# Kernel tuning notes

Hardware: AMD Instinct MI355X
Metric: run time of the kernel (lower is better)

The kernel has to match this reference:

```python
import jax, jax.numpy as jnp
import numpy as np

W_BIT = 4
G_SIZE = 128
HID = 4096
INTER = 11008
TOKS = (2, 2048)


def _dequant(qw, qz, scales, g_size):
    """Unpack int4 nibbles from int32 and dequantize: (w - zero) * scale.
    qw: [K, N//8] int32, qz: [K//g, N//8] int32, scales: [K//g, N] float.
    Returns dense weight [K, N] in scales.dtype."""
    K = qw.shape[0]
    shifts = (jnp.arange(8, dtype=jnp.int32) * 4)  # 8 nibbles per int32
    w = ((qw[:, :, None] >> shifts) & 0xF).reshape(K, -1).astype(scales.dtype)   # [K, N]
    z = ((qz[:, :, None] >> shifts) & 0xF).reshape(qz.shape[0], -1).astype(scales.dtype)  # [K//g, N]
    zr = jnp.repeat(z, g_size, axis=0)       # broadcast zero-points over group rows
    sr = jnp.repeat(scales, g_size, axis=0)  # broadcast scales over group rows
    return (w - zr) * sr


def setup_inputs() -> dict:
    key = jax.random.key(0)
    ks = jax.random.split(key, 7)
    B, S = TOKS
    x = jax.random.normal(ks[0], (B, S, HID), dtype=jnp.float32)
    imax = 2147483647
    qweight_gu = jax.random.randint(ks[1], (HID, 2 * INTER // 8), 0, imax, dtype=jnp.int32)
    qzeros_gu = jax.random.randint(ks[2], (HID // G_SIZE, 2 * INTER // 8), 0, imax, dtype=jnp.int32)
    scales_gu = jax.random.uniform(ks[3], (HID // G_SIZE, 2 * INTER), dtype=jnp.float32) * 0.01 + 1e-3
    qweight_dn = jax.random.randint(ks[4], (INTER, HID // 8), 0, imax, dtype=jnp.int32)
    qzeros_dn = jax.random.randint(ks[5], (INTER // G_SIZE, HID // 8), 0, imax, dtype=jnp.int32)
    scales_dn = jax.random.uniform(ks[6], (INTER // G_SIZE, HID), dtype=jnp.float32) * 0.01 + 1e-3
    return {"x": x, "qweight_gu": qweight_gu, "qzeros_gu": qzeros_gu, "scales_gu": scales_gu,
            "qweight_dn": qweight_dn, "qzeros_dn": qzeros_dn, "scales_dn": scales_dn}


def reference(x, qweight_gu, qzeros_gu, scales_gu, qweight_dn, qzeros_dn, scales_dn):
    # gate_up projection: x [B,S,H] @ W_gu [H, 2*I]
    W_gu = _dequant(qweight_gu, qzeros_gu, scales_gu, G_SIZE)
    gate_up = jnp.einsum('bsh,hi->bsi', x, W_gu)
    d = gate_up.shape[-1] // 2
    # SiluAndMul: silu(gate) * up
    h = jax.nn.silu(gate_up[..., :d]) * gate_up[..., d:]
    # down projection: h [B,S,I] @ W_dn [I, H]
    W_dn = _dequant(qweight_dn, qzeros_dn, scales_dn, G_SIZE)
    return jnp.einsum('bsi,ih->bsh', h, W_dn)
```

## Files before the change

kernel.cpp:

```cpp
#include <hip/hip_runtime.h>
#include <hip/hip_bf16.h>
#include <cstdint>
#include <cstddef>

#define AS1 __attribute__((address_space(1)))
#define AS3 __attribute__((address_space(3)))

constexpr int HIDC   = 4096;
constexpr int INTERC = 11008;
constexpr int NTOKC  = 4096;
constexpr int NWGU   = 2 * INTERC;

using f32x4 = __attribute__((ext_vector_type(4))) float;
using s16x8 = __attribute__((ext_vector_type(8))) short;

__device__ __forceinline__ short f2bf(float f) {
  __hip_bfloat16 h = __float2bfloat16(f);
  return __builtin_bit_cast(short, h);
}


__global__ void cvt_x_kernel(const float4* __restrict__ x, ushort4* __restrict__ xb, int n4) {
  int stride = gridDim.x * blockDim.x;
  for (int i = blockIdx.x * blockDim.x + threadIdx.x; i < n4; i += stride) {
    float4 v = x[i];
    ushort4 o;
    o.x = (unsigned short)f2bf(v.x);
    o.y = (unsigned short)f2bf(v.y);
    o.z = (unsigned short)f2bf(v.z);
    o.w = (unsigned short)f2bf(v.w);
    xb[i] = o;
  }
}

__global__ void repack_kernel(const uint32_t* __restrict__ qw, uint32_t* __restrict__ qt,
                              int kints, int Wn) {
  long total  = (long)Wn * kints;
  long stride = (long)gridDim.x * blockDim.x;
  for (long idx = blockIdx.x * (long)blockDim.x + threadIdx.x; idx < total; idx += stride) {
    int col = (int)(idx / kints);
    int kk  = (int)(idx - (long)col * kints);
    uint32_t ow[8] = {0, 0, 0, 0, 0, 0, 0, 0};
#pragma unroll
    for (int j = 0; j < 8; ++j) {
      uint32_t v = qw[(size_t)(kk * 8 + j) * Wn + col];
#pragma unroll
      for (int jn = 0; jn < 8; ++jn)
        ow[jn] |= ((v >> (4 * jn)) & 0xFu) << (4 * j);
    }
#pragma unroll
    for (int jn = 0; jn < 8; ++jn)
      qt[(size_t)(col * 8 + jn) * kints + kk] = ow[jn];
  }
}

__global__ void mktab_kernel(const uint32_t* __restrict__ qz, const float* __restrict__ sc,
                             float2* __restrict__ tab, int total, int Nw) {
  int stride = gridDim.x * blockDim.x;
  for (int idx = blockIdx.x * blockDim.x + threadIdx.x; idx < total; idx += stride) {
    int g = idx / Nw, n = idx - g * Nw;
    uint32_t z = (qz[(size_t)g * (Nw >> 3) + (n >> 3)] >> ((n & 7) * 4)) & 0xFu;
    float s = sc[idx];
    tab[idx] = make_float2(s, -s * (float)z);
  }
}

template <int DUAL, int KSTEPS, int KINTS, int NWTOT>
__global__ __launch_bounds__(256, 2) void qgemm_kernel(
    const __hip_bfloat16* __restrict__ A, const uint32_t* __restrict__ QT,
    const float2* __restrict__ TAB, __hip_bfloat16* __restrict__ Hout,
    float* __restrict__ Fout) {
  constexpr int K  = KSTEPS * 64;
  constexpr int NI = DUAL ? 2 : 4;
  __shared__ __align__(16) char lds[32768];

  const int tid  = threadIdx.x;
  const int lane = tid & 63;
  const int w    = tid >> 6;
  const int wr   = w >> 1, wc = w & 1;
  const int fr   = lane & 15;
  const int fq   = lane >> 4;
  const int nt   = blockIdx.x, mt = blockIdx.y;
  const int row0 = mt * 128;

  int a_src[4];
#pragma unroll
  for (int i = 0; i < 4; ++i) {
    int o = i * 4096 + tid * 16;
    int r = o >> 7;
    int b = (o & 127) ^ ((r & 7) << 4);
    a_src[i] = (row0 + r) * K + (b >> 1);
  }

  int s_mat, s_nl, s_kh, s_nglob;
  if (DUAL) {
    s_mat = tid >> 7;
    int tt = tid & 127;
    s_nl  = tt >> 1;
    s_kh  = tt & 1;
    s_nglob = nt * 64 + s_nl + (s_mat ? INTERC : 0);
  } else {
    s_mat = 0;
    s_nl  = tid >> 1;
    s_kh  = tid & 1;
    s_nglob = nt * 128 + s_nl;
  }
  char* bdst = lds + 16384 + s_mat * 8192 + s_nl * 128;
  const int bswz = (s_nl & 7) << 4;

  f32x4 acc0[4][NI] = {};
  f32x4 acc1[4][NI] = {};

#pragma unroll 1
  for (int kt = 0; kt < KSTEPS; ++kt) {
    if (kt) __syncthreads();

#pragma unroll
    for (int i = 0; i < 4; ++i) {
      const __hip_bfloat16* src = A + a_src[i] + kt * 64;
      __builtin_amdgcn_global_load_lds((const AS1 uint32_t*)src,
                                       (AS3 uint32_t*)(lds + i * 4096 + w * 1024),
                                       16, 0, 0);
    }

    {
      const int g = kt >> 1;
      const uint32_t* qp = QT + (size_t)s_nglob * KINTS + kt * 8 + s_kh * 4;
      uint4 q = *(const uint4*)qp;
      float2 sz = TAB[(size_t)g * NWTOT + s_nglob];
      uint32_t qq[4] = {q.x, q.y, q.z, q.w};
#pragma unroll
      for (int ii = 0; ii < 4; ++ii) {
        s16x8 wv;
#pragma unroll
        for (int j = 0; j < 8; ++j) {
          float v = (float)((qq[ii] >> (4 * j)) & 0xFu);
          wv[j] = f2bf(fmaf(v, sz.x, sz.y));
        }
        *(s16x8*)(bdst + ((s_kh * 64 + ii * 16) ^ bswz)) = wv;
      }
    }
    __syncthreads();

#pragma unroll
    for (int kk = 0; kk < 2; ++kk) {
      const int bb = (((kk << 2) | fq) ^ (fr & 7)) << 4;
      s16x8 av[4];
#pragma unroll
      for (int mi = 0; mi < 4; ++mi)
        av[mi] = *(const s16x8*)(lds + (wr * 64 + mi * 16 + fr) * 128 + bb);
      if (DUAL) {
#pragma unroll
        for (int ni = 0; ni < 2; ++ni) {
          const int brow = (wc * 32 + ni * 16 + fr) * 128 + bb;
          s16x8 bg = *(const s16x8*)(lds + 16384 + brow);
          s16x8 bu = *(const s16x8*)(lds + 24576 + brow);
#pragma unroll
          for (int mi = 0; mi < 4; ++mi) {
            acc0[mi][ni] = __builtin_amdgcn_mfma_f32_16x16x32_bf16(av[mi], bg, acc0[mi][ni], 0, 0, 0);
            acc1[mi][ni] = __builtin_amdgcn_mfma_f32_16x16x32_bf16(av[mi], bu, acc1[mi][ni], 0, 0, 0);
          }
        }
      } else {
#pragma unroll
        for (int ni = 0; ni < 4; ++ni) {
          s16x8 bv = *(const s16x8*)(lds + 16384 + (wc * 64 + ni * 16 + fr) * 128 + bb);
#pragma unroll
          for (int mi = 0; mi < 4; ++mi)
            acc0[mi][ni] = __builtin_amdgcn_mfma_f32_16x16x32_bf16(av[mi], bv, acc0[mi][ni], 0, 0, 0);
        }
      }
    }
  }

  if (DUAL) {
    const int col0 = nt * 64 + wc * 32;
#pragma unroll
    for (int mi = 0; mi < 4; ++mi) {
      const int rr = row0 + wr * 64 + mi * 16 + fq * 4;
#pragma unroll
      for (int ni = 0; ni < NI; ++ni) {
        const int cc = col0 + ni * 16 + fr;
#pragma unroll
        for (int r = 0; r < 4; ++r) {
          float gv = acc0[mi][ni][r];
          float uv = acc1[mi][ni][r];
          float hv = gv / (1.0f + __expf(-gv)) * uv;
          Hout[(size_t)(rr + r) * INTERC + cc] = __float2bfloat16(hv);
        }
      }
    }
  } else {
    const int col0 = nt * 128 + wc * 64;
#pragma unroll
    for (int mi = 0; mi < 4; ++mi) {
      const int rr = row0 + wr * 64 + mi * 16 + fq * 4;
#pragma unroll
      for (int ni = 0; ni < NI; ++ni) {
        const int cc = col0 + ni * 16 + fr;
#pragma unroll
        for (int r = 0; r < 4; ++r)
          Fout[(size_t)(rr + r) * HIDC + cc] = acc0[mi][ni][r];
      }
    }
  }
}

extern "C" void kernel_launch(void* const* d_in, const int* in_sizes, int n_in,
                              void* d_out, int out_size, void* d_ws, size_t ws_size,
                              hipStream_t stream) {
  const float*    x     = (const float*)d_in[0];
  const uint32_t* qw_gu = (const uint32_t*)d_in[1];
  const uint32_t* qz_gu = (const uint32_t*)d_in[2];
  const float*    sc_gu = (const float*)d_in[3];
  const uint32_t* qw_dn = (const uint32_t*)d_in[4];
  const uint32_t* qz_dn = (const uint32_t*)d_in[5];
  const float*    sc_dn = (const float*)d_in[6];
  float* out = (float*)d_out;

  char* ws = (char*)d_ws;
  __hip_bfloat16* xb   = (__hip_bfloat16*)(ws + 0);
  uint32_t*       qtgu = (uint32_t*)(ws + 33554432);
  uint32_t*       qtdn = (uint32_t*)(ws + 78643200);
  float2*         tgu  = (float2*)(ws + 101187584);
  float2*         tdn  = (float2*)(ws + 106823680);
  __hip_bfloat16* hbuf = (__hip_bfloat16*)(ws + 109641728);

  cvt_x_kernel<<<2048, 256, 0, stream>>>((const float4*)x, (ushort4*)xb, NTOKC * HIDC / 4);
  repack_kernel<<<2048, 256, 0, stream>>>(qw_gu, qtgu, HIDC / 8, NWGU / 8);
  repack_kernel<<<2048, 256, 0, stream>>>(qw_dn, qtdn, INTERC / 8, HIDC / 8);
  mktab_kernel<<<1024, 256, 0, stream>>>(qz_gu, sc_gu, tgu, (HIDC / 128) * NWGU, NWGU);
  mktab_kernel<<<1024, 256, 0, stream>>>(qz_dn, sc_dn, tdn, (INTERC / 128) * HIDC, HIDC);

  qgemm_kernel<1, 64, 512, NWGU>
      <<<dim3(INTERC / 64, NTOKC / 128), 256, 0, stream>>>(xb, qtgu, tgu, hbuf, nullptr);
  qgemm_kernel<0, 172, 1376, HIDC>
      <<<dim3(HIDC / 128, NTOKC / 128), 256, 0, stream>>>(hbuf, qtdn, tdn, nullptr, out);
}
```

Before: 1.323 ms.

## Switch GEMMs to fp16 with magic-number packed int4 dequantization

Moves activations, the intermediate buffer and the dequantized weights from bf16 to fp16 and uses the f16 MFMA. The repack now interleaves nibbles so that each 32-bit word can be split into packed half2 pairs with the 0x6400 magic-exponent trick. Dequantization then becomes a half2 subtract and a half2 fma, replacing eight scalar int-to-float conversions, fmas and bf16 conversions per word. The scale/zero table is stored as duplicated half2 pairs. The aim is to cut VALU cost in the B-tile dequant path. The cost is fp16 range limits: the intermediate h values or the scale times zero term could overflow or lose precision.

```diff
diff --git a/kernel.cpp b/kernel.cpp
--- a/kernel.cpp
+++ b/kernel.cpp
@@ -1,5 +1,6 @@
 #include <hip/hip_runtime.h>
 #include <hip/hip_bf16.h>
+#include <hip/hip_fp16.h>
 #include <cstdint>
 #include <cstddef>
 
@@ -12,24 +13,19 @@
 constexpr int NWGU   = 2 * INTERC;
 
 using f32x4 = __attribute__((ext_vector_type(4))) float;
-using s16x8 = __attribute__((ext_vector_type(8))) short;
-
-__device__ __forceinline__ short f2bf(float f) {
-  __hip_bfloat16 h = __float2bfloat16(f);
-  return __builtin_bit_cast(short, h);
-}
-
-
-__global__ void cvt_x_kernel(const float4* __restrict__ x, ushort4* __restrict__ xb, int n4) {
+using f16x8 = __attribute__((ext_vector_type(8))) _Float16;
+
+
+__global__ void cvt_x_kernel(const float4* __restrict__ x, ushort4* __restrict__ xh, int n4) {
   int stride = gridDim.x * blockDim.x;
   for (int i = blockIdx.x * blockDim.x + threadIdx.x; i < n4; i += stride) {
     float4 v = x[i];
     ushort4 o;
-    o.x = (unsigned short)f2bf(v.x);
-    o.y = (unsigned short)f2bf(v.y);
-    o.z = (unsigned short)f2bf(v.z);
-    o.w = (unsigned short)f2bf(v.w);
-    xb[i] = o;
+    o.x = __builtin_bit_cast(unsigned short, __float2half(v.x));
+    o.y = __builtin_bit_cast(unsigned short, __float2half(v.y));
+    o.z = __builtin_bit_cast(unsigned short, __float2half(v.z));
+    o.w = __builtin_bit_cast(unsigned short, __float2half(v.w));
+    xh[i] = o;
   }
 }
 
@@ -44,9 +40,10 @@
 #pragma unroll
     for (int j = 0; j < 8; ++j) {
       uint32_t v = qw[(size_t)(kk * 8 + j) * Wn + col];
+      const int pos = (j & 1) ? (4 + (j >> 1)) : (j >> 1);
 #pragma unroll
       for (int jn = 0; jn < 8; ++jn)
-        ow[jn] |= ((v >> (4 * jn)) & 0xFu) << (4 * j);
+        ow[jn] |= ((v >> (4 * jn)) & 0xFu) << (4 * pos);
     }
 #pragma unroll
     for (int jn = 0; jn < 8; ++jn)
@@ -55,20 +52,22 @@
 }
 
 __global__ void mktab_kernel(const uint32_t* __restrict__ qz, const float* __restrict__ sc,
-                             float2* __restrict__ tab, int total, int Nw) {
+                             uint2* __restrict__ tab, int total, int Nw) {
   int stride = gridDim.x * blockDim.x;
   for (int idx = blockIdx.x * blockDim.x + threadIdx.x; idx < total; idx += stride) {
     int g = idx / Nw, n = idx - g * Nw;
     uint32_t z = (qz[(size_t)g * (Nw >> 3) + (n >> 3)] >> ((n & 7) * 4)) & 0xFu;
     float s = sc[idx];
-    tab[idx] = make_float2(s, -s * (float)z);
+    uint32_t us = (uint32_t)__builtin_bit_cast(unsigned short, __float2half(s));
+    uint32_t uc = (uint32_t)__builtin_bit_cast(unsigned short, __float2half(-s * (float)z));
+    tab[idx] = make_uint2(us | (us << 16), uc | (uc << 16));
   }
 }
 
 template <int DUAL, int KSTEPS, int KINTS, int NWTOT>
 __global__ __launch_bounds__(256, 2) void qgemm_kernel(
-    const __hip_bfloat16* __restrict__ A, const uint32_t* __restrict__ QT,
-    const float2* __restrict__ TAB, __hip_bfloat16* __restrict__ Hout,
+    const __half* __restrict__ A, const uint32_t* __restrict__ QT,
+    const uint2* __restrict__ TAB, __half* __restrict__ Hout,
     float* __restrict__ Fout) {
   constexpr int K  = KSTEPS * 64;
   constexpr int NI = DUAL ? 2 : 4;
@@ -117,27 +116,32 @@
 
 #pragma unroll
     for (int i = 0; i < 4; ++i) {
-      const __hip_bfloat16* src = A + a_src[i] + kt * 64;
+      const __half* src = A + a_src[i] + kt * 64;
       __builtin_amdgcn_global_load_lds((const AS1 uint32_t*)src,
                                        (AS3 uint32_t*)(lds + i * 4096 + w * 1024),
                                        16, 0, 0);
     }
 
     {
-      const int g = kt >> 1;
       const uint32_t* qp = QT + (size_t)s_nglob * KINTS + kt * 8 + s_kh * 4;
       uint4 q = *(const uint4*)qp;
-      float2 sz = TAB[(size_t)g * NWTOT + s_nglob];
+      uint2 tz = TAB[(size_t)(kt >> 1) * NWTOT + s_nglob];
+      const __half2 s2 = __builtin_bit_cast(__half2, tz.x);
+      const __half2 c2 = __builtin_bit_cast(__half2, tz.y);
+      const __half2 k1024 = __builtin_bit_cast(__half2, 0x64006400u);
       uint32_t qq[4] = {q.x, q.y, q.z, q.w};
 #pragma unroll
-      for (int ii = 0; ii < 4; ++ii) {
-        s16x8 wv;
-#pragma unroll
-        for (int j = 0; j < 8; ++j) {
-          float v = (float)((qq[ii] >> (4 * j)) & 0xFu);
-          wv[j] = f2bf(fmaf(v, sz.x, sz.y));
-        }
-        *(s16x8*)(bdst + ((s_kh * 64 + ii * 16) ^ bswz)) = wv;
+      for (int p = 0; p < 4; ++p) {
+        uint32_t r_[4];
+#pragma unroll
+        for (int i = 0; i < 4; ++i) {
+          uint32_t pr = ((qq[p] >> (4 * i)) & 0x000F000Fu) | 0x64006400u;
+          __half2 t  = __hsub2(__builtin_bit_cast(__half2, pr), k1024);
+          __half2 wv = __hfma2(t, s2, c2);
+          r_[i] = __builtin_bit_cast(uint32_t, wv);
+        }
+        *(uint4*)(bdst + ((s_kh * 64 + p * 16) ^ bswz)) =
+            make_uint4(r_[0], r_[1], r_[2], r_[3]);
       }
     }
     __syncthreads();
@@ -145,29 +149,29 @@
 #pragma unroll
     for (int kk = 0; kk < 2; ++kk) {
       const int bb = (((kk << 2) | fq) ^ (fr & 7)) << 4;
-      s16x8 av[4];
+      f16x8 av[4];
 #pragma unroll
       for (int mi = 0; mi < 4; ++mi)
-        av[mi] = *(const s16x8*)(lds + (wr * 64 + mi * 16 + fr) * 128 + bb);
+        av[mi] = *(const f16x8*)(lds + (wr * 64 + mi * 16 + fr) * 128 + bb);
       if (DUAL) {
 #pragma unroll
         for (int ni = 0; ni < 2; ++ni) {
           const int brow = (wc * 32 + ni * 16 + fr) * 128 + bb;
-          s16x8 bg = *(const s16x8*)(lds + 16384 + brow);
-          s16x8 bu = *(const s16x8*)(lds + 24576 + brow);
+          f16x8 bg = *(const f16x8*)(lds + 16384 + brow);
+          f16x8 bu = *(const f16x8*)(lds + 24576 + brow);
 #pragma unroll
           for (int mi = 0; mi < 4; ++mi) {
-            acc0[mi][ni] = __builtin_amdgcn_mfma_f32_16x16x32_bf16(av[mi], bg, acc0[mi][ni], 0, 0, 0);
-            acc1[mi][ni] = __builtin_amdgcn_mfma_f32_16x16x32_bf16(av[mi], bu, acc1[mi][ni], 0, 0, 0);
+            acc0[mi][ni] = __builtin_amdgcn_mfma_f32_16x16x32_f16(av[mi], bg, acc0[mi][ni], 0, 0, 0);
+            acc1[mi][ni] = __builtin_amdgcn_mfma_f32_16x16x32_f16(av[mi], bu, acc1[mi][ni], 0, 0, 0);
           }
         }
       } else {
 #pragma unroll
         for (int ni = 0; ni < 4; ++ni) {
-          s16x8 bv = *(const s16x8*)(lds + 16384 + (wc * 64 + ni * 16 + fr) * 128 + bb);
+          f16x8 bv = *(const f16x8*)(lds + 16384 + (wc * 64 + ni * 16 + fr) * 128 + bb);
 #pragma unroll
           for (int mi = 0; mi < 4; ++mi)
-            acc0[mi][ni] = __builtin_amdgcn_mfma_f32_16x16x32_bf16(av[mi], bv, acc0[mi][ni], 0, 0, 0);
+            acc0[mi][ni] = __builtin_amdgcn_mfma_f32_16x16x32_f16(av[mi], bv, acc0[mi][ni], 0, 0, 0);
         }
       }
     }
@@ -186,7 +190,7 @@
           float gv = acc0[mi][ni][r];
           float uv = acc1[mi][ni][r];
           float hv = gv / (1.0f + __expf(-gv)) * uv;
-          Hout[(size_t)(rr + r) * INTERC + cc] = __float2bfloat16(hv);
+          Hout[(size_t)(rr + r) * INTERC + cc] = __float2half(hv);
         }
       }
     }
@@ -219,21 +223,21 @@
   float* out = (float*)d_out;
 
   char* ws = (char*)d_ws;
-  __hip_bfloat16* xb   = (__hip_bfloat16*)(ws + 0);
-  uint32_t*       qtgu = (uint32_t*)(ws + 33554432);
-  uint32_t*       qtdn = (uint32_t*)(ws + 78643200);
-  float2*         tgu  = (float2*)(ws + 101187584);
-  float2*         tdn  = (float2*)(ws + 106823680);
-  __hip_bfloat16* hbuf = (__hip_bfloat16*)(ws + 109641728);
-
-  cvt_x_kernel<<<2048, 256, 0, stream>>>((const float4*)x, (ushort4*)xb, NTOKC * HIDC / 4);
+  __half*   xh   = (__half*)(ws + 0);
+  uint32_t* qtgu = (uint32_t*)(ws + 33554432);
+  uint32_t* qtdn = (uint32_t*)(ws + 78643200);
+  uint2*    tgu  = (uint2*)(ws + 101187584);
+  uint2*    tdn  = (uint2*)(ws + 106823680);
+  __half*   hbuf = (__half*)(ws + 109641728);
+
+  cvt_x_kernel<<<2048, 256, 0, stream>>>((const float4*)x, (ushort4*)xh, NTOKC * HIDC / 4);
   repack_kernel<<<2048, 256, 0, stream>>>(qw_gu, qtgu, HIDC / 8, NWGU / 8);
   repack_kernel<<<2048, 256, 0, stream>>>(qw_dn, qtdn, INTERC / 8, HIDC / 8);
   mktab_kernel<<<1024, 256, 0, stream>>>(qz_gu, sc_gu, tgu, (HIDC / 128) * NWGU, NWGU);
   mktab_kernel<<<1024, 256, 0, stream>>>(qz_dn, sc_dn, tdn, (INTERC / 128) * HIDC, HIDC);
 
   qgemm_kernel<1, 64, 512, NWGU>
-      <<<dim3(INTERC / 64, NTOKC / 128), 256, 0, stream>>>(xb, qtgu, tgu, hbuf, nullptr);
+      <<<dim3(INTERC / 64, NTOKC / 128), 256, 0, stream>>>(xh, qtgu, tgu, hbuf, nullptr);
   qgemm_kernel<0, 172, 1376, HIDC>
       <<<dim3(HIDC / 128, NTOKC / 128), 256, 0, stream>>>(hbuf, qtdn, tdn, nullptr, out);
 }
```

New measurement: 1.300 ms. About the same (-1.7%).
